# Kernel optimization log

Hardware: AMD Instinct MI355X
Metric: run time of the kernel (lower is better)

The kernel has to match this reference:

```python
import jax, jax.numpy as jnp
import numpy as np


def g(x):
    # mingru activation: x+0.5 for x>=0, sigmoid(x) otherwise (g(0)=0.5)
    return jnp.where(x >= 0, x + 0.5, jax.nn.sigmoid(x))


def setup_inputs() -> dict:
    key = jax.random.key(0)
    k1, k2, k3 = jax.random.split(key, 3)
    x = jax.random.normal(k1, (8, 64, 16, 64, 64), jnp.float32)      # (B,S,C,H,W)
    W = jax.random.normal(k2, (64, 16, 3, 3), jnp.float32) * 0.05    # (2*outd, ind, k, k)
    b = jax.random.normal(k3, (64,), jnp.float32) * 0.05
    return {"x": x, "W": W, "b": b}


def reference(x, W, b):
    B, S, C, H, Wd = x.shape
    out_ch = W.shape[0] // 2
    # conv per timestep: fold S into batch, VALID padding (Conv2d default padding=0)
    y = jax.lax.conv_general_dilated(
        x.reshape(B * S, C, H, Wd), W, window_strides=(1, 1), padding='VALID',
        dimension_numbers=('NCHW', 'OIHW', 'NCHW'))
    y = y + b[None, :, None, None]
    Hp, Wp = y.shape[-2], y.shape[-1]
    y = y.reshape(B, S, 2 * out_ch, Hp, Wp)
    gate = y[:, :, :out_ch]
    hidden = y[:, :, out_ch:]

    # minGRU: h_t = (1 - z_t) * h_{t-1} + z_t * g(hhat_t),  z_t = sigmoid(gate_t)
    z = jax.nn.sigmoid(gate)
    coeff = 1.0 - z                # multiplier on h_{t-1}
    val = z * g(hidden)            # additive term
    h0 = jnp.full((B, out_ch, Hp, Wp), 0.5, x.dtype)  # g(zeros) initial state
    val = val.at[:, 0].add(coeff[:, 0] * h0)

    def combine(a, b_):
        ca, va = a
        cb, vb = b_
        return (ca * cb, va * cb + vb)

    _, h = jax.lax.associative_scan(combine, (coeff, val), axis=1)  # (B,S,outd,Hp,Wp)
    h_final = h[:, -1:][None]  # (num_layers=1, B, 1, outd, Hp, Wp)
    return h, h_final
```

## Files before the change

### kernel.cpp

```cpp
#include <hip/hip_runtime.h>
#include <hip/hip_bf16.h>

namespace {

typedef __attribute__((ext_vector_type(8))) short bf16x8;
typedef __attribute__((ext_vector_type(4))) float f32x4;

constexpr int kB = 8, kS = 64, kC = 16, kH = 64, kW = 64;
constexpr int kHC = 32, kHP = 62, kWP = 62;
constexpr int kPlane = kH * kW * kC;
constexpr int kPix = kHP * kWP;
constexpr int kKpad = 160;

__global__ __launch_bounds__(256)
void transpose_x(const float* __restrict__ x, __hip_bfloat16* __restrict__ xt)
{
    const size_t idx = (size_t)blockIdx.x * 256 + threadIdx.x;
    const size_t bs  = idx >> 12;
    const int    px  = (int)(idx & 4095);
    const float* src = x + bs * (size_t)(kC * kH * kW) + px;

    float v[16];
    #pragma unroll
    for (int ic = 0; ic < 16; ++ic) v[ic] = src[ic * (kH * kW)];

    union { unsigned short u[16]; uint4 q[2]; } p;
    #pragma unroll
    for (int ic = 0; ic < 16; ++ic) {
        __hip_bfloat16 hb = __float2bfloat16(v[ic]);
        p.u[ic] = *reinterpret_cast<unsigned short*>(&hb);
    }
    uint4* dst = reinterpret_cast<uint4*>(xt + idx * 16);
    dst[0] = p.q[0];
    dst[1] = p.q[1];
}

__global__ __launch_bounds__(256)
void reorder_w(const float* __restrict__ wgt, __hip_bfloat16* __restrict__ wk)
{
    const int i = blockIdx.x * 256 + threadIdx.x;
    if (i >= 64 * kKpad) return;
    const int oc = i / kKpad, k = i % kKpad;
    float val = 0.f;
    if (k < 144) {
        const int ky = k / 48, r = k % 48, kx = r / 16, ic = r % 16;
        val = wgt[oc * 144 + ic * 9 + ky * 3 + kx];
    }
    wk[i] = __float2bfloat16(val);
}

__global__ __launch_bounds__(256, 2)
void conv_gru_mfma(const __hip_bfloat16* __restrict__ xt,
                   const __hip_bfloat16* __restrict__ wk,
                   const float* __restrict__ bias,
                   float* __restrict__ out)
{
    const int tid  = threadIdx.x;
    const int lane = tid & 63;
    const int wv   = tid >> 6;
    const int py   = blockIdx.x;
    const int b    = blockIdx.y;
    const int px0  = wv * 16;
    const int n    = lane & 15;
    const int q    = lane >> 4;

    bf16x8 wf[4][5];
    #pragma unroll
    for (int t = 0; t < 4; ++t)
        #pragma unroll
        for (int c = 0; c < 5; ++c)
            wf[t][c] = *reinterpret_cast<const bf16x8*>(
                wk + (t * 16 + n) * kKpad + c * 32 + q * 8);

    const int m = n;
    const int px_eff = (px0 + m > 61) ? 61 : (px0 + m);
    int aoff[5];
    #pragma unroll
    for (int c = 0; c < 5; ++c) {
        int k = c * 32 + q * 8;
        int ky, off;
        if (k >= 144) { ky = 2; off = 32; }
        else          { ky = k / 48; off = k % 48; }
        aoff[c] = (py + ky) * (kW * kC) + px_eff * kC + off;
    }

    const __hip_bfloat16* xb = xt + (size_t)b * kS * kPlane;

    const float bg[2] = { bias[n],      bias[16 + n] };
    const float bh[2] = { bias[32 + n], bias[48 + n] };

    float h[2][4];
    #pragma unroll
    for (int t = 0; t < 2; ++t)
        #pragma unroll
        for (int r = 0; r < 4; ++r) h[t][r] = 0.5f;

    float* outh = out + (size_t)b * kS * kHC * kPix;
    float* outf = out + (size_t)kB * kS * kHC * kPix + (size_t)b * kHC * kPix;

    const int px_st = px0 + q * 4;
    const bool full4 = (px_st + 3 <= 61);

    for (int s = 0; s < kS; ++s) {
        const __hip_bfloat16* xs = xb + (size_t)s * kPlane;

        bf16x8 af[5];
        #pragma unroll
        for (int c = 0; c < 5; ++c)
            af[c] = *reinterpret_cast<const bf16x8*>(xs + aoff[c]);

        f32x4 acc[4];
        #pragma unroll
        for (int t = 0; t < 4; ++t) acc[t] = (f32x4){0.f, 0.f, 0.f, 0.f};

        #pragma unroll
        for (int c = 0; c < 5; ++c)
            #pragma unroll
            for (int t = 0; t < 4; ++t)
                acc[t] = __builtin_amdgcn_mfma_f32_16x16x32_bf16(af[c], wf[t][c], acc[t], 0, 0, 0);

        float* os = outh + (size_t)s * kHC * kPix + py * kWP;
        #pragma unroll
        for (int t = 0; t < 2; ++t) {
            #pragma unroll
            for (int r = 0; r < 4; ++r) {
                const float gate = acc[t][r]     + bg[t];
                const float hid  = acc[t + 2][r] + bh[t];
                const float z    = 1.f / (1.f + __expf(-gate));
                const float gv   = (hid >= 0.f) ? (hid + 0.5f)
                                                : 1.f / (1.f + __expf(-hid));
                h[t][r] = (1.f - z) * h[t][r] + z * gv;
            }
            float* p = os + (t * 16 + n) * kPix + px_st;
            if (full4) {
                *reinterpret_cast<float4*>(p) = make_float4(h[t][0], h[t][1], h[t][2], h[t][3]);
            } else {
                #pragma unroll
                for (int r = 0; r < 4; ++r)
                    if (px_st + r <= 61) p[r] = h[t][r];
            }
            if (s == kS - 1) {
                float* pf = outf + (t * 16 + n) * kPix + py * kWP + px_st;
                if (full4) {
                    *reinterpret_cast<float4*>(pf) = make_float4(h[t][0], h[t][1], h[t][2], h[t][3]);
                } else {
                    #pragma unroll
                    for (int r = 0; r < 4; ++r)
                        if (px_st + r <= 61) pf[r] = h[t][r];
                }
            }
        }
    }
}

}

extern "C" void kernel_launch(void* const* d_in, const int* in_sizes, int n_in,
                              void* d_out, int out_size, void* d_ws, size_t ws_size,
                              hipStream_t stream)
{
    const float* x  = (const float*)d_in[0];
    const float* Wt = (const float*)d_in[1];
    const float* b  = (const float*)d_in[2];
    float* out = (float*)d_out;

    __hip_bfloat16* wk = (__hip_bfloat16*)d_ws;
    __hip_bfloat16* xt = (__hip_bfloat16*)((char*)d_ws + 32768);

    reorder_w<<<dim3((64 * kKpad + 255) / 256), dim3(256), 0, stream>>>(Wt, wk);
    transpose_x<<<dim3(kB * kS * kH * kW / 256), dim3(256), 0, stream>>>(x, xt);
    conv_gru_mfma<<<dim3(kHP, kB), dim3(256), 0, stream>>>(xt, wk, b, out);
}
```

Baseline: 486.3 us.

## Split conv-GRU over channel halves, double-buffer input loads, vectorize transpose

The transpose kernel now has each thread handle four pixels, using float4 loads and eight 16-byte stores. The conv-GRU grid gains a z dimension that splits the 32 hidden channels into two groups, doubling the block count and halving per-thread accumulators and weight registers, with launch bounds raised to 4. The time loop is unrolled by two with a software-prefetched input buffer so the next step's loads overlap the current MFMAs. Outputs use nontemporal stores, the sigmoid uses a fast reciprocal, and the final-state write moves out of the loop. In exchange, each input tile is loaded twice, once per channel group.

```diff
diff --git a/kernel.cpp b/kernel.cpp
--- a/kernel.cpp
+++ b/kernel.cpp
@@ -15,24 +15,29 @@
 __global__ __launch_bounds__(256)
 void transpose_x(const float* __restrict__ x, __hip_bfloat16* __restrict__ xt)
 {
-    const size_t idx = (size_t)blockIdx.x * 256 + threadIdx.x;
-    const size_t bs  = idx >> 12;
-    const int    px  = (int)(idx & 4095);
-    const float* src = x + bs * (size_t)(kC * kH * kW) + px;
+    const size_t gi = (size_t)blockIdx.x * 256 + threadIdx.x;
+    const size_t bs = gi >> 10;
+    const int px0 = ((int)gi & 1023) << 2;
+    const float* src = x + bs * (size_t)kPlane + px0;
 
-    float v[16];
+    float4 v[16];
     #pragma unroll
-    for (int ic = 0; ic < 16; ++ic) v[ic] = src[ic * (kH * kW)];
+    for (int ic = 0; ic < 16; ++ic)
+        v[ic] = *reinterpret_cast<const float4*>(src + (size_t)ic * (kH * kW));
 
-    union { unsigned short u[16]; uint4 q[2]; } p;
+    union { unsigned short u[8]; uint4 q; } pk[8];
     #pragma unroll
-    for (int ic = 0; ic < 16; ++ic) {
-        __hip_bfloat16 hb = __float2bfloat16(v[ic]);
-        p.u[ic] = *reinterpret_cast<unsigned short*>(&hb);
+    for (int p = 0; p < 4; ++p) {
+        #pragma unroll
+        for (int ic = 0; ic < 16; ++ic) {
+            const float f = reinterpret_cast<const float*>(&v[ic])[p];
+            __hip_bfloat16 hb = __float2bfloat16(f);
+            pk[p * 2 + (ic >> 3)].u[ic & 7] = *reinterpret_cast<unsigned short*>(&hb);
+        }
     }
-    uint4* dst = reinterpret_cast<uint4*>(xt + idx * 16);
-    dst[0] = p.q[0];
-    dst[1] = p.q[1];
+    uint4* dst = reinterpret_cast<uint4*>(xt + (bs * 4096 + (size_t)px0) * 16);
+    #pragma unroll
+    for (int j = 0; j < 8; ++j) dst[j] = pk[j].q;
 }
 
 __global__ __launch_bounds__(256)
@@ -49,7 +54,7 @@
     wk[i] = __float2bfloat16(val);
 }
 
-__global__ __launch_bounds__(256, 2)
+__global__ __launch_bounds__(256, 4)
 void conv_gru_mfma(const __hip_bfloat16* __restrict__ xt,
                    const __hip_bfloat16* __restrict__ wk,
                    const float* __restrict__ bias,
@@ -60,20 +65,19 @@
     const int wv   = tid >> 6;
     const int py   = blockIdx.x;
     const int b    = blockIdx.y;
+    const int t    = blockIdx.z;
     const int px0  = wv * 16;
     const int n    = lane & 15;
     const int q    = lane >> 4;
 
-    bf16x8 wf[4][5];
+    bf16x8 wfG[5], wfH[5];
     #pragma unroll
-    for (int t = 0; t < 4; ++t)
-        #pragma unroll
-        for (int c = 0; c < 5; ++c)
-            wf[t][c] = *reinterpret_cast<const bf16x8*>(
-                wk + (t * 16 + n) * kKpad + c * 32 + q * 8);
+    for (int c = 0; c < 5; ++c) {
+        wfG[c] = *reinterpret_cast<const bf16x8*>(wk + (t * 16 + n) * kKpad + c * 32 + q * 8);
+        wfH[c] = *reinterpret_cast<const bf16x8*>(wk + ((t + 2) * 16 + n) * kKpad + c * 32 + q * 8);
+    }
 
-    const int m = n;
-    const int px_eff = (px0 + m > 61) ? 61 : (px0 + m);
+    const int px_eff = (px0 + n > 61) ? 61 : (px0 + n);
     int aoff[5];
     #pragma unroll
     for (int c = 0; c < 5; ++c) {
@@ -85,71 +89,76 @@
     }
 
     const __hip_bfloat16* xb = xt + (size_t)b * kS * kPlane;
+    const float bg = bias[t * 16 + n];
+    const float bh = bias[32 + t * 16 + n];
 
-    const float bg[2] = { bias[n],      bias[16 + n] };
-    const float bh[2] = { bias[32 + n], bias[48 + n] };
-
-    float h[2][4];
-    #pragma unroll
-    for (int t = 0; t < 2; ++t)
-        #pragma unroll
-        for (int r = 0; r < 4; ++r) h[t][r] = 0.5f;
-
-    float* outh = out + (size_t)b * kS * kHC * kPix;
-    float* outf = out + (size_t)kB * kS * kHC * kPix + (size_t)b * kHC * kPix;
+    float h[4] = {0.5f, 0.5f, 0.5f, 0.5f};
 
     const int px_st = px0 + q * 4;
     const bool full4 = (px_st + 3 <= 61);
 
-    for (int s = 0; s < kS; ++s) {
-        const __hip_bfloat16* xs = xb + (size_t)s * kPlane;
+    float* op = out + (size_t)b * kS * kHC * kPix
+                    + (size_t)(t * 16 + n) * kPix + (size_t)py * kWP + px_st;
+    constexpr size_t sStride = (size_t)kHC * kPix;
 
-        bf16x8 af[5];
+    auto step = [&](const bf16x8 (&af)[5], float* p) {
+        f32x4 a0 = {0.f, 0.f, 0.f, 0.f}, a1 = {0.f, 0.f, 0.f, 0.f};
         #pragma unroll
-        for (int c = 0; c < 5; ++c)
-            af[c] = *reinterpret_cast<const bf16x8*>(xs + aoff[c]);
+        for (int c = 0; c < 5; ++c) {
+            a0 = __builtin_amdgcn_mfma_f32_16x16x32_bf16(af[c], wfG[c], a0, 0, 0, 0);
+            a1 = __builtin_amdgcn_mfma_f32_16x16x32_bf16(af[c], wfH[c], a1, 0, 0, 0);
+        }
+        #pragma unroll
+        for (int r = 0; r < 4; ++r) {
+            const float gate = a0[r] + bg;
+            const float hid  = a1[r] + bh;
+            const float z  = __builtin_amdgcn_rcpf(1.f + __expf(-gate));
+            const float sg = __builtin_amdgcn_rcpf(1.f + __expf(-hid));
+            const float gv = (hid >= 0.f) ? (hid + 0.5f) : sg;
+            h[r] += z * (gv - h[r]);
+        }
+        if (full4) {
+            f32x4 hv = {h[0], h[1], h[2], h[3]};
+            __builtin_nontemporal_store(hv, reinterpret_cast<f32x4*>(p));
+        } else {
+            #pragma unroll
+            for (int r = 0; r < 4; ++r)
+                if (px_st + r <= 61) __builtin_nontemporal_store(h[r], p + r);
+        }
+    };
 
-        f32x4 acc[4];
+    bf16x8 afA[5], afB[5];
+    #pragma unroll
+    for (int c = 0; c < 5; ++c)
+        afA[c] = *reinterpret_cast<const bf16x8*>(xb + aoff[c]);
+
+    for (int s = 0; s < kS; s += 2) {
+        {
+            const __hip_bfloat16* xn = xb + (size_t)(s + 1) * kPlane;
+            #pragma unroll
+            for (int c = 0; c < 5; ++c)
+                afB[c] = *reinterpret_cast<const bf16x8*>(xn + aoff[c]);
+            step(afA, op + (size_t)s * sStride);
+        }
+        {
+            const int sp = (s + 2 < kS) ? (s + 2) : (kS - 1);
+            const __hip_bfloat16* xn = xb + (size_t)sp * kPlane;
+            #pragma unroll
+            for (int c = 0; c < 5; ++c)
+                afA[c] = *reinterpret_cast<const bf16x8*>(xn + aoff[c]);
+            step(afB, op + (size_t)(s + 1) * sStride);
+        }
+    }
+
+    float* pf = out + (size_t)kB * kS * kHC * kPix + (size_t)b * kHC * kPix
+                    + (size_t)(t * 16 + n) * kPix + (size_t)py * kWP + px_st;
+    if (full4) {
+        f32x4 hv = {h[0], h[1], h[2], h[3]};
+        __builtin_nontemporal_store(hv, reinterpret_cast<f32x4*>(pf));
+    } else {
         #pragma unroll
-        for (int t = 0; t < 4; ++t) acc[t] = (f32x4){0.f, 0.f, 0.f, 0.f};
-
-        #pragma unroll
-        for (int c = 0; c < 5; ++c)
-            #pragma unroll
-            for (int t = 0; t < 4; ++t)
-                acc[t] = __builtin_amdgcn_mfma_f32_16x16x32_bf16(af[c], wf[t][c], acc[t], 0, 0, 0);
-
-        float* os = outh + (size_t)s * kHC * kPix + py * kWP;
-        #pragma unroll
-        for (int t = 0; t < 2; ++t) {
-            #pragma unroll
-            for (int r = 0; r < 4; ++r) {
-                const float gate = acc[t][r]     + bg[t];
-                const float hid  = acc[t + 2][r] + bh[t];
-                const float z    = 1.f / (1.f + __expf(-gate));
-                const float gv   = (hid >= 0.f) ? (hid + 0.5f)
-                                                : 1.f / (1.f + __expf(-hid));
-                h[t][r] = (1.f - z) * h[t][r] + z * gv;
-            }
-            float* p = os + (t * 16 + n) * kPix + px_st;
-            if (full4) {
-                *reinterpret_cast<float4*>(p) = make_float4(h[t][0], h[t][1], h[t][2], h[t][3]);
-            } else {
-                #pragma unroll
-                for (int r = 0; r < 4; ++r)
-                    if (px_st + r <= 61) p[r] = h[t][r];
-            }
-            if (s == kS - 1) {
-                float* pf = outf + (t * 16 + n) * kPix + py * kWP + px_st;
-                if (full4) {
-                    *reinterpret_cast<float4*>(pf) = make_float4(h[t][0], h[t][1], h[t][2], h[t][3]);
-                } else {
-                    #pragma unroll
-                    for (int r = 0; r < 4; ++r)
-                        if (px_st + r <= 61) pf[r] = h[t][r];
-                }
-            }
-        }
+        for (int r = 0; r < 4; ++r)
+            if (px_st + r <= 61) __builtin_nontemporal_store(h[r], pf + r);
     }
 }
 
@@ -168,6 +177,6 @@
     __hip_bfloat16* xt = (__hip_bfloat16*)((char*)d_ws + 32768);
 
     reorder_w<<<dim3((64 * kKpad + 255) / 256), dim3(256), 0, stream>>>(Wt, wk);
-    transpose_x<<<dim3(kB * kS * kH * kW / 256), dim3(256), 0, stream>>>(x, xt);
-    conv_gru_mfma<<<dim3(kHP, kB), dim3(256), 0, stream>>>(xt, wk, b, out);
+    transpose_x<<<dim3(kB * kS * kH * kW / 4 / 256), dim3(256), 0, stream>>>(x, xt);
+    conv_gru_mfma<<<dim3(kHP, kB, 2), dim3(256), 0, stream>>>(xt, wk, b, out);
 }
```

Measured after the change: 655.7 us. +34.8%, slower.

## Vectorize transpose, double-buffer timestep loads, remap grid, simplify GRU math

Applied to the files above, without the earlier changes.

The transpose kernel now handles four pixels per thread, using float4 loads and eight 16-byte stores, and launches a quarter as many threads. The conv-GRU kernel flattens its grid so that the batch index varies fastest. It also double-buffers the input fragments, loading timestep s+1 while the MFMAs for step s run, so global-load latency is hidden. The gating uses hardware reciprocal intrinsics in place of divisions, computes the sigmoid of the hidden term unconditionally, and rewrites the recurrence as h += z*(g-h). The extra fragment buffer raises register pressure, and the approximate reciprocal slightly changes numerics.

```diff
diff --git a/kernel.cpp b/kernel.cpp
--- a/kernel.cpp
+++ b/kernel.cpp
@@ -15,24 +15,29 @@
 __global__ __launch_bounds__(256)
 void transpose_x(const float* __restrict__ x, __hip_bfloat16* __restrict__ xt)
 {
-    const size_t idx = (size_t)blockIdx.x * 256 + threadIdx.x;
-    const size_t bs  = idx >> 12;
-    const int    px  = (int)(idx & 4095);
-    const float* src = x + bs * (size_t)(kC * kH * kW) + px;
+    const size_t gi = (size_t)blockIdx.x * 256 + threadIdx.x;
+    const size_t bs = gi >> 10;
+    const int px0 = ((int)gi & 1023) << 2;
+    const float* src = x + bs * (size_t)kPlane + px0;
 
-    float v[16];
+    float4 v[16];
     #pragma unroll
-    for (int ic = 0; ic < 16; ++ic) v[ic] = src[ic * (kH * kW)];
+    for (int ic = 0; ic < 16; ++ic)
+        v[ic] = *reinterpret_cast<const float4*>(src + (size_t)ic * (kH * kW));
 
-    union { unsigned short u[16]; uint4 q[2]; } p;
+    union { unsigned short u[8]; uint4 q; } pk[8];
     #pragma unroll
-    for (int ic = 0; ic < 16; ++ic) {
-        __hip_bfloat16 hb = __float2bfloat16(v[ic]);
-        p.u[ic] = *reinterpret_cast<unsigned short*>(&hb);
+    for (int p = 0; p < 4; ++p) {
+        #pragma unroll
+        for (int ic = 0; ic < 16; ++ic) {
+            const float f = reinterpret_cast<const float*>(&v[ic])[p];
+            __hip_bfloat16 hb = __float2bfloat16(f);
+            pk[p * 2 + (ic >> 3)].u[ic & 7] = *reinterpret_cast<unsigned short*>(&hb);
+        }
     }
-    uint4* dst = reinterpret_cast<uint4*>(xt + idx * 16);
-    dst[0] = p.q[0];
-    dst[1] = p.q[1];
+    uint4* dst = reinterpret_cast<uint4*>(xt + (bs * 4096 + (size_t)px0) * 16);
+    #pragma unroll
+    for (int j = 0; j < 8; ++j) dst[j] = pk[j].q;
 }
 
 __global__ __launch_bounds__(256)
@@ -58,8 +63,9 @@
     const int tid  = threadIdx.x;
     const int lane = tid & 63;
     const int wv   = tid >> 6;
-    const int py   = blockIdx.x;
-    const int b    = blockIdx.y;
+    const int lin  = blockIdx.x;
+    const int b    = lin & 7;
+    const int py   = lin >> 3;
     const int px0  = wv * 16;
     const int n    = lane & 15;
     const int q    = lane >> 4;
@@ -69,11 +75,10 @@
     for (int t = 0; t < 4; ++t)
         #pragma unroll
         for (int c = 0; c < 5; ++c)
-            wf[t][c] = *reinterpret_cast<const bf16x8*>(
+            wf[t][c] = *reinterpret_cast<const volatile bf16x8*>(
                 wk + (t * 16 + n) * kKpad + c * 32 + q * 8);
 
-    const int m = n;
-    const int px_eff = (px0 + m > 61) ? 61 : (px0 + m);
+    const int px_eff = (px0 + n > 61) ? 61 : (px0 + n);
     int aoff[5];
     #pragma unroll
     for (int c = 0; c < 5; ++c) {
@@ -85,7 +90,6 @@
     }
 
     const __hip_bfloat16* xb = xt + (size_t)b * kS * kPlane;
-
     const float bg[2] = { bias[n],      bias[16 + n] };
     const float bh[2] = { bias[32 + n], bias[48 + n] };
 
@@ -95,20 +99,14 @@
         #pragma unroll
         for (int r = 0; r < 4; ++r) h[t][r] = 0.5f;
 
-    float* outh = out + (size_t)b * kS * kHC * kPix;
-    float* outf = out + (size_t)kB * kS * kHC * kPix + (size_t)b * kHC * kPix;
-
     const int px_st = px0 + q * 4;
     const bool full4 = (px_st + 3 <= 61);
 
-    for (int s = 0; s < kS; ++s) {
-        const __hip_bfloat16* xs = xb + (size_t)s * kPlane;
+    float* outh = out + (size_t)b * kS * kHC * kPix + (size_t)py * kWP;
+    float* outf = out + (size_t)kB * kS * kHC * kPix + (size_t)b * kHC * kPix
+                      + (size_t)py * kWP;
 
-        bf16x8 af[5];
-        #pragma unroll
-        for (int c = 0; c < 5; ++c)
-            af[c] = *reinterpret_cast<const bf16x8*>(xs + aoff[c]);
-
+    auto step = [&](const bf16x8 (&af)[5], int s) {
         f32x4 acc[4];
         #pragma unroll
         for (int t = 0; t < 4; ++t) acc[t] = (f32x4){0.f, 0.f, 0.f, 0.f};
@@ -119,17 +117,17 @@
             for (int t = 0; t < 4; ++t)
                 acc[t] = __builtin_amdgcn_mfma_f32_16x16x32_bf16(af[c], wf[t][c], acc[t], 0, 0, 0);
 
-        float* os = outh + (size_t)s * kHC * kPix + py * kWP;
+        float* os = outh + (size_t)s * (kHC * kPix);
         #pragma unroll
         for (int t = 0; t < 2; ++t) {
             #pragma unroll
             for (int r = 0; r < 4; ++r) {
                 const float gate = acc[t][r]     + bg[t];
                 const float hid  = acc[t + 2][r] + bh[t];
-                const float z    = 1.f / (1.f + __expf(-gate));
-                const float gv   = (hid >= 0.f) ? (hid + 0.5f)
-                                                : 1.f / (1.f + __expf(-hid));
-                h[t][r] = (1.f - z) * h[t][r] + z * gv;
+                const float z  = __builtin_amdgcn_rcpf(1.f + __expf(-gate));
+                const float sg = __builtin_amdgcn_rcpf(1.f + __expf(-hid));
+                const float gv = (hid >= 0.f) ? (hid + 0.5f) : sg;
+                h[t][r] += z * (gv - h[t][r]);
             }
             float* p = os + (t * 16 + n) * kPix + px_st;
             if (full4) {
@@ -140,7 +138,7 @@
                     if (px_st + r <= 61) p[r] = h[t][r];
             }
             if (s == kS - 1) {
-                float* pf = outf + (t * 16 + n) * kPix + py * kWP + px_st;
+                float* pf = outf + (t * 16 + n) * kPix + px_st;
                 if (full4) {
                     *reinterpret_cast<float4*>(pf) = make_float4(h[t][0], h[t][1], h[t][2], h[t][3]);
                 } else {
@@ -150,6 +148,26 @@
                 }
             }
         }
+    };
+
+    bf16x8 afA[5], afB[5];
+    #pragma unroll
+    for (int c = 0; c < 5; ++c)
+        afA[c] = *reinterpret_cast<const bf16x8*>(xb + aoff[c]);
+
+    for (int s = 0; s < kS; s += 2) {
+        const __hip_bfloat16* x1 = xb + (size_t)(s + 1) * kPlane;
+        #pragma unroll
+        for (int c = 0; c < 5; ++c)
+            afB[c] = *reinterpret_cast<const bf16x8*>(x1 + aoff[c]);
+        step(afA, s);
+
+        const int sp = (s + 2 < kS) ? (s + 2) : (kS - 1);
+        const __hip_bfloat16* x2 = xb + (size_t)sp * kPlane;
+        #pragma unroll
+        for (int c = 0; c < 5; ++c)
+            afA[c] = *reinterpret_cast<const bf16x8*>(x2 + aoff[c]);
+        step(afB, s + 1);
     }
 }
 
@@ -168,6 +186,6 @@
     __hip_bfloat16* xt = (__hip_bfloat16*)((char*)d_ws + 32768);
 
     reorder_w<<<dim3((64 * kKpad + 255) / 256), dim3(256), 0, stream>>>(Wt, wk);
-    transpose_x<<<dim3(kB * kS * kH * kW / 256), dim3(256), 0, stream>>>(x, xt);
-    conv_gru_mfma<<<dim3(kHP, kB), dim3(256), 0, stream>>>(xt, wk, b, out);
+    transpose_x<<<dim3(kB * kS * kH * kW / 4 / 256), dim3(256), 0, stream>>>(x, xt);
+    conv_gru_mfma<<<dim3(kHP * kB), dim3(256), 0, stream>>>(xt, wk, b, out);
 }
```

After: 483.2 us. About the same (-0.6%).
